# Performance work log

Measured on AMD Instinct MI355X. Metric: run time of the kernel, lower is better.

The kernel has to match this reference:

```python
import jax, jax.numpy as jnp
import numpy as np

N, M, D = 256, 64, 1024


def _l2norm(x, axis=-1, eps=1e-12):
    # tf.math.l2_normalize semantics: x / sqrt(max(sum(x^2), eps))
    sq = jnp.sum(x * x, axis=axis, keepdims=True)
    return x * jax.lax.rsqrt(jnp.maximum(sq, eps))


def setup_inputs() -> dict:
    key = jax.random.key(0)
    k1, = jax.random.split(key, 1)
    inputs = jax.random.normal(k1, (N * M, D), dtype=jnp.float32)
    w = jnp.full((1,), 10.0, dtype=jnp.float32)
    b = jnp.full((1,), -5.0, dtype=jnp.float32)
    return {"inputs": inputs, "w": w, "b": b}


def reference(inputs, w, b):
    emb = inputs.reshape(N, M, D)                       # (N, M, D)
    # speaker centroids (normalized mean over utterances)
    center = _l2norm(jnp.mean(emb, axis=1))             # (N, D)
    # leave-one-out centroid per utterance: sum over M minus self (NOT divided)
    center_except = _l2norm(jnp.sum(emb, axis=1, keepdims=True) - emb)  # (N, M, D)
    # off-diagonal similarities: every utterance vs every speaker centroid
    sim_all = jnp.einsum('jmd,id->jmi', emb, center)    # (N_utt_spk j, M, N_centroid i)
    # diagonal (i == j): utterance vs its own leave-one-out centroid
    diag = jnp.sum(center_except * emb, axis=-1)        # (N, M)
    eye = jnp.eye(N, dtype=bool)[:, None, :]            # (N, 1, N)
    sim = jnp.where(eye, diag[:, :, None], sim_all)     # (N, M, N)
    sim = w * sim + b
    return sim.reshape(N * M, N)
```

## Files before the change

### kernel.cpp

```cpp
#include <hip/hip_runtime.h>

#define NSPK 256
#define MUTT 64
#define DDIM 1024
#define NROW (NSPK * MUTT)

using frag_ab = __attribute__((ext_vector_type(8))) short;
using frag_cd = __attribute__((ext_vector_type(4))) float;

static __device__ __forceinline__ unsigned short f32_to_bf16(float f) {
    unsigned int u = __float_as_uint(f);
    return (unsigned short)((u + 0x7FFFu + ((u >> 16) & 1u)) >> 16);
}
static __device__ __forceinline__ unsigned int pack2(float a, float b) {
    return (unsigned)f32_to_bf16(a) | ((unsigned)f32_to_bf16(b) << 16);
}
static __device__ __forceinline__ void gload16(const void* g, void* l) {
    __builtin_amdgcn_global_load_lds(
        (const __attribute__((address_space(1))) unsigned int*)g,
        (__attribute__((address_space(3))) unsigned int*)l, 16, 0, 0);
}


__global__ void __launch_bounds__(512) k_prep(const float* __restrict__ emb,
                                              unsigned short* __restrict__ ebf,
                                              unsigned short* __restrict__ cbf,
                                              float* __restrict__ qg,
                                              float* __restrict__ n2g,
                                              float* __restrict__ n1g) {
    const int j = blockIdx.x;
    const int t = threadIdx.x;
    const int cg = t & 255;
    const int half = t >> 8;
    const int lane = t & 63, wave = t >> 6;
    const size_t rb = (size_t)j * MUTT + (size_t)half * 32;
    const float* src = emb + rb * DDIM + (size_t)cg * 4;
    unsigned short* edst = ebf + rb * DDIM + (size_t)cg * 4;
    __shared__ float qws[64][4];
    __shared__ float4 csum[256];
    __shared__ float red[4];
    __shared__ float sc_sh;
    float4 s = make_float4(0.f, 0.f, 0.f, 0.f);
    #pragma unroll 8
    for (int m = 0; m < 32; ++m) {
        float4 v = *(const float4*)(src + (size_t)m * DDIM);
        s.x += v.x; s.y += v.y; s.z += v.z; s.w += v.w;
        float qp = v.x * v.x + v.y * v.y + v.z * v.z + v.w * v.w;
        #pragma unroll
        for (int off = 32; off > 0; off >>= 1) qp += __shfl_down(qp, off, 64);
        if (lane == 0) qws[half * 32 + m][wave & 3] = qp;
        *(uint2*)(edst + (size_t)m * DDIM) = make_uint2(pack2(v.x, v.y), pack2(v.z, v.w));
    }
    if (half) csum[cg] = s;
    __syncthreads();
    if (t < 64) qg[(size_t)j * MUTT + t] = qws[t][0] + qws[t][1] + qws[t][2] + qws[t][3];
    if (!half) {
        float4 c = csum[cg];
        s.x += c.x; s.y += c.y; s.z += c.z; s.w += c.w;
        float sq = s.x * s.x + s.y * s.y + s.z * s.z + s.w * s.w;
        #pragma unroll
        for (int off = 32; off > 0; off >>= 1) sq += __shfl_down(sq, off, 64);
        if (lane == 0) red[wave] = sq;
    }
    __syncthreads();
    if (t == 0) {
        float tot = red[0] + red[1] + red[2] + red[3];
        n2g[j] = tot;
        n1g[j] = sqrtf(tot);
        float msq = tot * (1.0f / 4096.0f);
        sc_sh = rsqrtf(fmaxf(msq, 1e-12f)) * (1.0f / 64.0f);
    }
    __syncthreads();
    if (!half) {
        const float sc = sc_sh;
        *(uint2*)(cbf + (size_t)j * DDIM + (size_t)cg * 4) =
            make_uint2(pack2(s.x * sc, s.y * sc), pack2(s.z * sc, s.w * sc));
    }
}

__global__ void __launch_bounds__(256)
k_gemm(const unsigned short* __restrict__ ebf, const unsigned short* __restrict__ cbf,
       const float* __restrict__ qg, const float* __restrict__ n2g,
       const float* __restrict__ n1g,
       const float* __restrict__ wp, const float* __restrict__ bp,
       float* __restrict__ out) {
    __shared__ unsigned short lds[2 * 32768];

    const int tid = threadIdx.x, lane = tid & 63, wave = tid >> 6;
    const int rt = blockIdx.x;
    const int ct = blockIdx.y;
    const int row0 = rt * 128, c0 = ct * 128;

    int goff[8];
    #pragma unroll
    for (int i = 0; i < 8; ++i) {
        int c = i * 256 + tid, row = c >> 4, sw = c & 15;
        goff[i] = row * (DDIM * 2) + ((sw ^ (row & 15)) << 4);
    }
    const int stsh = wave * 512;
    const char* ag = (const char*)(ebf + (size_t)row0 * DDIM);
    const char* bg = (const char*)(cbf + (size_t)c0 * DDIM);

    const int quad = lane >> 4, m16 = lane & 15;
    const int wrow = wave >> 1, wcol = wave & 1;

    frag_cd acc[4][4];
    #pragma unroll
    for (int rr = 0; rr < 4; ++rr)
        #pragma unroll
        for (int cc = 0; cc < 4; ++cc) acc[rr][cc] = (frag_cd){0.f, 0.f, 0.f, 0.f};

    #pragma unroll
    for (int i = 0; i < 8; ++i) gload16(ag + goff[i], &lds[i * 2048 + stsh]);
    #pragma unroll
    for (int i = 0; i < 8; ++i) gload16(bg + goff[i], &lds[16384 + i * 2048 + stsh]);
    __syncthreads();

    const int NIT = DDIM / 128;
    for (int it = 0; it < NIT; ++it) {
        const int cur = it & 1;
        if (it + 1 < NIT) {
            const char* an = ag + (size_t)(it + 1) * 256;
            const char* bn = bg + (size_t)(it + 1) * 256;
            unsigned short* Ln = &lds[(cur ^ 1) * 32768];
            #pragma unroll
            for (int i = 0; i < 8; ++i) gload16(an + goff[i], Ln + i * 2048 + stsh);
            #pragma unroll
            for (int i = 0; i < 8; ++i) gload16(bn + goff[i], Ln + 16384 + i * 2048 + stsh);
        }
        const unsigned short* L = &lds[cur * 32768];
        #pragma unroll
        for (int s = 0; s < 4; ++s) {
            const int kc = (s << 2) + quad;
            frag_ab af[4], bf4[4];
            #pragma unroll
            for (int rr = 0; rr < 4; ++rr) {
                int r = wrow * 64 + rr * 16 + m16;
                int addr = r * 256 + ((kc ^ (r & 15)) << 4);
                af[rr] = *(const frag_ab*)&L[addr >> 1];
            }
            #pragma unroll
            for (int cc = 0; cc < 4; ++cc) {
                int r = wcol * 64 + cc * 16 + m16;
                int addr = 32768 + r * 256 + ((kc ^ (r & 15)) << 4);
                bf4[cc] = *(const frag_ab*)&L[addr >> 1];
            }
            #pragma unroll
            for (int rr = 0; rr < 4; ++rr)
                #pragma unroll
                for (int cc = 0; cc < 4; ++cc)
                    acc[rr][cc] = __builtin_amdgcn_mfma_f32_16x16x32_bf16(
                        af[rr], bf4[cc], acc[rr][cc], 0, 0, 0);
        }
        __syncthreads();
    }

    const float wv = wp[0], bv = bp[0];
    #pragma unroll
    for (int rr = 0; rr < 4; ++rr) {
        int rbase = wrow * 64 + rr * 16 + (quad << 2);
        #pragma unroll
        for (int cc = 0; cc < 4; ++cc) {
            int col = c0 + wcol * 64 + cc * 16 + m16;
            frag_cd v = acc[rr][cc];
            #pragma unroll
            for (int r2 = 0; r2 < 4; ++r2) {
                int grow = row0 + rbase + r2;
                float val = v[r2];
                int js = grow >> 6;
                if (col == js) {
                    float q = qg[grow];
                    float rd = val * n1g[js];
                    float den2 = n2g[js] - 2.f * rd + q;
                    val = (rd - q) * rsqrtf(fmaxf(den2, 1e-12f));
                }
                out[(size_t)grow * NSPK + col] = wv * val + bv;
            }
        }
    }
}


__global__ void k_sums(const float* __restrict__ emb, float* __restrict__ Sp) {
    const int j = blockIdx.x;
    const int h = blockIdx.y;
    const int c = threadIdx.x;
    const float* base = emb + ((size_t)j * MUTT + (size_t)h * 32) * DDIM + (size_t)c * 4;
    float4 acc = make_float4(0.f, 0.f, 0.f, 0.f);
    #pragma unroll 8
    for (int m = 0; m < 32; ++m) {
        float4 v = *(const float4*)(base + (size_t)m * DDIM);
        acc.x += v.x; acc.y += v.y; acc.z += v.z; acc.w += v.w;
    }
    *(float4*)(Sp + ((size_t)h * NSPK + j) * DDIM + (size_t)c * 4) = acc;
}

template <int P>
__global__ void k_center(const float* __restrict__ Sp, unsigned short* __restrict__ cbf,
                         float* __restrict__ normS2g, float* __restrict__ normSg) {
    const int j = blockIdx.x;
    const int t = threadIdx.x;
    float4 v = make_float4(0.f, 0.f, 0.f, 0.f);
    #pragma unroll
    for (int p = 0; p < P; ++p) {
        float4 a = *(const float4*)(Sp + ((size_t)p * NSPK + j) * DDIM + (size_t)t * 4);
        v.x += a.x; v.y += a.y; v.z += a.z; v.w += a.w;
    }
    float sq = v.x * v.x + v.y * v.y + v.z * v.z + v.w * v.w;
    #pragma unroll
    for (int off = 32; off > 0; off >>= 1) sq += __shfl_down(sq, off, 64);
    __shared__ float ws[4];
    __shared__ float sc_sh;
    const int lane = t & 63, wave = t >> 6;
    if (lane == 0) ws[wave] = sq;
    __syncthreads();
    if (t == 0) {
        float tot = ws[0] + ws[1] + ws[2] + ws[3];
        normS2g[j] = tot;
        normSg[j]  = sqrtf(tot);
        float msq = tot * (1.0f / 4096.0f);
        sc_sh = rsqrtf(fmaxf(msq, 1e-12f)) * (1.0f / 64.0f);
    }
    __syncthreads();
    const float sc = sc_sh;
    *(uint2*)(cbf + (size_t)j * DDIM + (size_t)t * 4) =
        make_uint2(pack2(v.x * sc, v.y * sc), pack2(v.z * sc, v.w * sc));
}

__global__ void __launch_bounds__(256)
k_gemm_old(const float* __restrict__ emb, const unsigned short* __restrict__ cbf,
           const float* __restrict__ normS2g, const float* __restrict__ normSg,
           const float* __restrict__ wp, const float* __restrict__ bp,
           float* __restrict__ out) {
    __shared__ unsigned short Asm[32][32];
    __shared__ unsigned short Bsm[256][32];
    __shared__ float qpart[32][8];
    __shared__ float qfin[32];
    const int tid = threadIdx.x, lane = tid & 63, wave = tid >> 6;
    const int row0 = blockIdx.x * 32;
    const int jspk = row0 >> 6;
    frag_cd acc[2][4];
    #pragma unroll
    for (int rr = 0; rr < 2; ++rr)
        #pragma unroll
        for (int cc = 0; cc < 4; ++cc) acc[rr][cc] = (frag_cd){0.f, 0.f, 0.f, 0.f};
    const int ar = tid >> 3, ak = (tid & 7) << 2;
    const float* aptr = emb + (size_t)(row0 + ar) * DDIM + ak;
    float qacc = 0.f;
    const int bi = tid >> 2, bk = (tid & 3) << 3;
    const int am = lane & 15, kq = (lane >> 4) << 3;
    for (int k0 = 0; k0 < DDIM; k0 += 32) {
        __syncthreads();
        float4 av = *(const float4*)(aptr + k0);
        qacc += av.x * av.x + av.y * av.y + av.z * av.z + av.w * av.w;
        *(uint2*)&Asm[ar][ak] = make_uint2(pack2(av.x, av.y), pack2(av.z, av.w));
        #pragma unroll
        for (int p = 0; p < 4; ++p) {
            int brow = p * 64 + bi;
            *(uint4*)&Bsm[brow][bk] = *(const uint4*)(cbf + (size_t)brow * DDIM + k0 + bk);
        }
        __syncthreads();
        frag_ab afr[2], bfr[4];
        #pragma unroll
        for (int rr = 0; rr < 2; ++rr) afr[rr] = *(const frag_ab*)&Asm[rr * 16 + am][kq];
        #pragma unroll
        for (int cc = 0; cc < 4; ++cc) bfr[cc] = *(const frag_ab*)&Bsm[wave * 64 + cc * 16 + am][kq];
        #pragma unroll
        for (int rr = 0; rr < 2; ++rr)
            #pragma unroll
            for (int cc = 0; cc < 4; ++cc)
                acc[rr][cc] = __builtin_amdgcn_mfma_f32_16x16x32_bf16(afr[rr], bfr[cc], acc[rr][cc], 0, 0, 0);
    }
    qpart[ar][tid & 7] = qacc;
    __syncthreads();
    if (tid < 32) {
        float s = 0.f;
        #pragma unroll
        for (int u = 0; u < 8; ++u) s += qpart[tid][u];
        qfin[tid] = s;
    }
    __syncthreads();
    const float wv = wp[0], bv = bp[0];
    const float ns2 = normS2g[jspk], ns = normSg[jspk];
    #pragma unroll
    for (int rr = 0; rr < 2; ++rr) {
        int rbase = rr * 16 + ((lane >> 4) << 2);
        #pragma unroll
        for (int cc = 0; cc < 4; ++cc) {
            int col = wave * 64 + cc * 16 + (lane & 15);
            frag_cd v = acc[rr][cc];
            #pragma unroll
            for (int r2 = 0; r2 < 4; ++r2) {
                int lrow = rbase + r2;
                float val = v[r2];
                if (col == jspk) {
                    float q = qfin[lrow];
                    float rd = val * ns;
                    float den2 = ns2 - 2.f * rd + q;
                    val = (rd - q) * rsqrtf(fmaxf(den2, 1e-12f));
                }
                out[(size_t)(row0 + lrow) * NSPK + col] = wv * val + bv;
            }
        }
    }
}

extern "C" void kernel_launch(void* const* d_in, const int* in_sizes, int n_in,
                              void* d_out, int out_size, void* d_ws, size_t ws_size,
                              hipStream_t stream) {
    const float* emb = (const float*)d_in[0];
    const float* w   = (const float*)d_in[1];
    const float* b   = (const float*)d_in[2];
    float* out = (float*)d_out;

    const size_t sz_ebf = (size_t)NROW * DDIM * 2;
    const size_t sz_cbf = (size_t)NSPK * DDIM * 2;
    const size_t sz_qg  = (size_t)NROW * 4;
    const size_t need = sz_ebf + sz_cbf + sz_qg + 2 * NSPK * 4;

    if (ws_size >= need) {
        char* p = (char*)d_ws;
        unsigned short* ebf = (unsigned short*)p; p += sz_ebf;
        unsigned short* cbf = (unsigned short*)p; p += sz_cbf;
        float* qg = (float*)p;                    p += sz_qg;
        float* n2 = (float*)p;
        float* n1 = n2 + NSPK;
        k_prep<<<NSPK, 512, 0, stream>>>(emb, ebf, cbf, qg, n2, n1);
        k_gemm<<<dim3(128, 2), 256, 0, stream>>>(ebf, cbf, qg, n2, n1, w, b, out);
    } else {
        float* Sp = (float*)d_ws;
        unsigned short* cbf = (unsigned short*)(Sp + 2 * NSPK * DDIM);
        float* n2 = (float*)(cbf + NSPK * DDIM);
        float* n1 = n2 + NSPK;
        k_sums<<<dim3(NSPK, 2), 256, 0, stream>>>(emb, Sp);
        k_center<2><<<NSPK, 256, 0, stream>>>(Sp, cbf, n2, n1);
        k_gemm_old<<<NROW / 32, 256, 0, stream>>>(emb, cbf, n2, n1, w, b, out);
    }
}
```

Baseline: 135.3 us.

## Fuse bf16 conversion of embeddings into GEMM and drop bf16 staging buffer

The prep kernel no longer writes a bf16 copy of the full embedding matrix. The GEMM now reads fp32 embeddings straight from global memory, converts them to bf16 in registers and writes them to LDS. It uses one block per speaker (64 rows × 256 columns) with 32x32x16 MFMAs and a three-stage register/LDS pipeline with explicit waitcnt. This removes a 32 MB bf16 write and its re-read, at the cost of GEMM blocks reading fp32 A (twice the bytes) and doing the conversion inside the main loop.

```diff
diff --git a/kernel.cpp b/kernel.cpp
--- a/kernel.cpp
+++ b/kernel.cpp
@@ -5,8 +5,9 @@
 #define DDIM 1024
 #define NROW (NSPK * MUTT)
 
-using frag_ab = __attribute__((ext_vector_type(8))) short;
-using frag_cd = __attribute__((ext_vector_type(4))) float;
+using frag_ab  = __attribute__((ext_vector_type(8)))  short;
+using frag_cd  = __attribute__((ext_vector_type(4)))  float;
+using frag_c16 = __attribute__((ext_vector_type(16))) float;
 
 static __device__ __forceinline__ unsigned short f32_to_bf16(float f) {
     unsigned int u = __float_as_uint(f);
@@ -22,12 +23,11 @@
 }
 
 
-__global__ void __launch_bounds__(512) k_prep(const float* __restrict__ emb,
-                                              unsigned short* __restrict__ ebf,
-                                              unsigned short* __restrict__ cbf,
-                                              float* __restrict__ qg,
-                                              float* __restrict__ n2g,
-                                              float* __restrict__ n1g) {
+__global__ void __launch_bounds__(512) k_prepc(const float* __restrict__ emb,
+                                               unsigned short* __restrict__ cbf,
+                                               float* __restrict__ qg,
+                                               float* __restrict__ n2g,
+                                               float* __restrict__ n1g) {
     const int j = blockIdx.x;
     const int t = threadIdx.x;
     const int cg = t & 255;
@@ -35,7 +35,6 @@
     const int lane = t & 63, wave = t >> 6;
     const size_t rb = (size_t)j * MUTT + (size_t)half * 32;
     const float* src = emb + rb * DDIM + (size_t)cg * 4;
-    unsigned short* edst = ebf + rb * DDIM + (size_t)cg * 4;
     __shared__ float qws[64][4];
     __shared__ float4 csum[256];
     __shared__ float red[4];
@@ -49,7 +48,6 @@
         #pragma unroll
         for (int off = 32; off > 0; off >>= 1) qp += __shfl_down(qp, off, 64);
         if (lane == 0) qws[half * 32 + m][wave & 3] = qp;
-        *(uint2*)(edst + (size_t)m * DDIM) = make_uint2(pack2(v.x, v.y), pack2(v.z, v.w));
     }
     if (half) csum[cg] = s;
     __syncthreads();
@@ -79,99 +77,121 @@
 }
 
 __global__ void __launch_bounds__(256)
-k_gemm(const unsigned short* __restrict__ ebf, const unsigned short* __restrict__ cbf,
-       const float* __restrict__ qg, const float* __restrict__ n2g,
-       const float* __restrict__ n1g,
-       const float* __restrict__ wp, const float* __restrict__ bp,
-       float* __restrict__ out) {
-    __shared__ unsigned short lds[2 * 32768];
+k_gemmf(const float* __restrict__ emb, const unsigned short* __restrict__ cbf,
+        const float* __restrict__ qg, const float* __restrict__ n2g,
+        const float* __restrict__ n1g,
+        const float* __restrict__ wp, const float* __restrict__ bp,
+        float* __restrict__ out) {
+    __shared__ unsigned short lds[3 * 20480];
 
     const int tid = threadIdx.x, lane = tid & 63, wave = tid >> 6;
-    const int rt = blockIdx.x;
-    const int ct = blockIdx.y;
-    const int row0 = rt * 128, c0 = ct * 128;
-
-    int goff[8];
-    #pragma unroll
-    for (int i = 0; i < 8; ++i) {
-        int c = i * 256 + tid, row = c >> 4, sw = c & 15;
-        goff[i] = row * (DDIM * 2) + ((sw ^ (row & 15)) << 4);
-    }
-    const int stsh = wave * 512;
-    const char* ag = (const char*)(ebf + (size_t)row0 * DDIM);
-    const char* bg = (const char*)(cbf + (size_t)c0 * DDIM);
-
-    const int quad = lane >> 4, m16 = lane & 15;
-    const int wrow = wave >> 1, wcol = wave & 1;
-
-    frag_cd acc[4][4];
-    #pragma unroll
-    for (int rr = 0; rr < 4; ++rr)
-        #pragma unroll
-        for (int cc = 0; cc < 4; ++cc) acc[rr][cc] = (frag_cd){0.f, 0.f, 0.f, 0.f};
-
-    #pragma unroll
-    for (int i = 0; i < 8; ++i) gload16(ag + goff[i], &lds[i * 2048 + stsh]);
-    #pragma unroll
-    for (int i = 0; i < 8; ++i) gload16(bg + goff[i], &lds[16384 + i * 2048 + stsh]);
-    __syncthreads();
-
-    const int NIT = DDIM / 128;
-    for (int it = 0; it < NIT; ++it) {
-        const int cur = it & 1;
-        if (it + 1 < NIT) {
-            const char* an = ag + (size_t)(it + 1) * 256;
-            const char* bn = bg + (size_t)(it + 1) * 256;
-            unsigned short* Ln = &lds[(cur ^ 1) * 32768];
-            #pragma unroll
-            for (int i = 0; i < 8; ++i) gload16(an + goff[i], Ln + i * 2048 + stsh);
-            #pragma unroll
-            for (int i = 0; i < 8; ++i) gload16(bn + goff[i], Ln + 16384 + i * 2048 + stsh);
-        }
-        const unsigned short* L = &lds[cur * 32768];
-        #pragma unroll
-        for (int s = 0; s < 4; ++s) {
-            const int kc = (s << 2) + quad;
-            frag_ab af[4], bf4[4];
-            #pragma unroll
-            for (int rr = 0; rr < 4; ++rr) {
-                int r = wrow * 64 + rr * 16 + m16;
-                int addr = r * 256 + ((kc ^ (r & 15)) << 4);
-                af[rr] = *(const frag_ab*)&L[addr >> 1];
+    const int j = blockIdx.x;
+    const int row0 = j * 64;
+
+    const int arow = tid >> 3;
+    const int ga = (tid & 7) ^ (arow & 7);
+    const float* ap0 = emb + (size_t)(row0 + arow) * DDIM + ga * 8;
+    const float* ap1 = ap0 + (size_t)32 * DDIM;
+
+    const int bbase = arow * DDIM + ga * 8;
+
+    const int l31 = lane & 31, l5 = lane >> 5;
+
+    frag_c16 acc[2][2];
+    #pragma unroll
+    for (int rr = 0; rr < 2; ++rr)
+        #pragma unroll
+        for (int cc = 0; cc < 2; ++cc)
+            #pragma unroll
+            for (int q = 0; q < 16; ++q) acc[rr][cc][q] = 0.f;
+
+    float4 rA[2][4];
+
+    auto issueS = [&](int t, float4 ra[4]) {
+        const int ko = t * 64;
+        ra[0] = *(const float4*)(ap0 + ko);
+        ra[1] = *(const float4*)(ap0 + ko + 4);
+        ra[2] = *(const float4*)(ap1 + ko);
+        ra[3] = *(const float4*)(ap1 + ko + 4);
+        unsigned short* LB = &lds[(t % 3) * 20480 + 4096];
+        #pragma unroll
+        for (int i = 0; i < 8; ++i)
+            gload16(cbf + (size_t)bbase + (size_t)i * 32 * DDIM + ko,
+                    LB + ((size_t)i * 256 + tid) * 8);
+    };
+    auto writeA = [&](int t, float4 ra[4]) {
+        unsigned short* LA = &lds[(t % 3) * 20480];
+        uint4 p0 = make_uint4(pack2(ra[0].x, ra[0].y), pack2(ra[0].z, ra[0].w),
+                              pack2(ra[1].x, ra[1].y), pack2(ra[1].z, ra[1].w));
+        uint4 p1 = make_uint4(pack2(ra[2].x, ra[2].y), pack2(ra[2].z, ra[2].w),
+                              pack2(ra[3].x, ra[3].y), pack2(ra[3].z, ra[3].w));
+        *(uint4*)&LA[(size_t)tid * 8] = p0;
+        *(uint4*)&LA[((size_t)tid + 256) * 8] = p1;
+    };
+
+    issueS(0, rA[0]);
+    issueS(1, rA[1]);
+    asm volatile("s_waitcnt vmcnt(12)" ::: "memory");
+    writeA(0, rA[0]);
+    asm volatile("s_waitcnt lgkmcnt(0)" ::: "memory");
+    __builtin_amdgcn_s_barrier();
+    __builtin_amdgcn_sched_barrier(0);
+
+    const int NIT = DDIM / 64;
+    #pragma unroll
+    for (int t = 0; t < NIT; ++t) {
+        if (t + 2 < NIT) issueS(t + 2, rA[t & 1]);
+
+        const unsigned short* L  = &lds[(t % 3) * 20480];
+        const unsigned short* LB = L + 4096;
+        #pragma unroll
+        for (int ks = 0; ks < 4; ++ks) {
+            const int kc = 2 * ks + l5;
+            frag_ab af[2], bfr[2];
+            #pragma unroll
+            for (int rr = 0; rr < 2; ++rr) {
+                int r = rr * 32 + l31;
+                af[rr] = *(const frag_ab*)&L[r * 64 + ((kc ^ (r & 7)) << 3)];
             }
             #pragma unroll
-            for (int cc = 0; cc < 4; ++cc) {
-                int r = wcol * 64 + cc * 16 + m16;
-                int addr = 32768 + r * 256 + ((kc ^ (r & 15)) << 4);
-                bf4[cc] = *(const frag_ab*)&L[addr >> 1];
+            for (int cc = 0; cc < 2; ++cc) {
+                int r = wave * 64 + cc * 32 + l31;
+                bfr[cc] = *(const frag_ab*)&LB[r * 64 + ((kc ^ (r & 7)) << 3)];
             }
             #pragma unroll
-            for (int rr = 0; rr < 4; ++rr)
+            for (int rr = 0; rr < 2; ++rr)
                 #pragma unroll
-                for (int cc = 0; cc < 4; ++cc)
-                    acc[rr][cc] = __builtin_amdgcn_mfma_f32_16x16x32_bf16(
-                        af[rr], bf4[cc], acc[rr][cc], 0, 0, 0);
-        }
-        __syncthreads();
+                for (int cc = 0; cc < 2; ++cc)
+                    acc[rr][cc] = __builtin_amdgcn_mfma_f32_32x32x16_bf16(
+                        af[rr], bfr[cc], acc[rr][cc], 0, 0, 0);
+        }
+
+        if (t < NIT - 1) {
+            if (t + 2 < NIT) asm volatile("s_waitcnt vmcnt(12)" ::: "memory");
+            else             asm volatile("s_waitcnt vmcnt(0)"  ::: "memory");
+            writeA(t + 1, rA[(t + 1) & 1]);
+            asm volatile("s_waitcnt lgkmcnt(0)" ::: "memory");
+            __builtin_amdgcn_s_barrier();
+            __builtin_amdgcn_sched_barrier(0);
+        }
     }
 
     const float wv = wp[0], bv = bp[0];
-    #pragma unroll
-    for (int rr = 0; rr < 4; ++rr) {
-        int rbase = wrow * 64 + rr * 16 + (quad << 2);
-        #pragma unroll
-        for (int cc = 0; cc < 4; ++cc) {
-            int col = c0 + wcol * 64 + cc * 16 + m16;
-            frag_cd v = acc[rr][cc];
-            #pragma unroll
-            for (int r2 = 0; r2 < 4; ++r2) {
-                int grow = row0 + rbase + r2;
-                float val = v[r2];
-                int js = grow >> 6;
-                if (col == js) {
+    const float ns2 = n2g[j], ns = n1g[j];
+    #pragma unroll
+    for (int rr = 0; rr < 2; ++rr) {
+        #pragma unroll
+        for (int cc = 0; cc < 2; ++cc) {
+            frag_c16 v = acc[rr][cc];
+            const int col = wave * 64 + cc * 32 + l31;
+            #pragma unroll
+            for (int r = 0; r < 16; ++r) {
+                int grow = row0 + rr * 32 + (r & 3) + 8 * (r >> 2) + 4 * l5;
+                float val = v[r];
+                if (col == j) {
                     float q = qg[grow];
-                    float rd = val * n1g[js];
-                    float den2 = n2g[js] - 2.f * rd + q;
+                    float rd = val * ns;
+                    float den2 = ns2 - 2.f * rd + q;
                     val = (rd - q) * rsqrtf(fmaxf(den2, 1e-12f));
                 }
                 out[(size_t)grow * NSPK + col] = wv * val + bv;
@@ -313,20 +333,18 @@
     const float* b   = (const float*)d_in[2];
     float* out = (float*)d_out;
 
-    const size_t sz_ebf = (size_t)NROW * DDIM * 2;
     const size_t sz_cbf = (size_t)NSPK * DDIM * 2;
     const size_t sz_qg  = (size_t)NROW * 4;
-    const size_t need = sz_ebf + sz_cbf + sz_qg + 2 * NSPK * 4;
+    const size_t need = sz_cbf + sz_qg + 2 * NSPK * 4;
 
     if (ws_size >= need) {
         char* p = (char*)d_ws;
-        unsigned short* ebf = (unsigned short*)p; p += sz_ebf;
         unsigned short* cbf = (unsigned short*)p; p += sz_cbf;
         float* qg = (float*)p;                    p += sz_qg;
         float* n2 = (float*)p;
         float* n1 = n2 + NSPK;
-        k_prep<<<NSPK, 512, 0, stream>>>(emb, ebf, cbf, qg, n2, n1);
-        k_gemm<<<dim3(128, 2), 256, 0, stream>>>(ebf, cbf, qg, n2, n1, w, b, out);
+        k_prepc<<<NSPK, 512, 0, stream>>>(emb, cbf, qg, n2, n1);
+        k_gemmf<<<NSPK, 256, 0, stream>>>(emb, cbf, qg, n2, n1, w, b, out);
     } else {
         float* Sp = (float*)d_ws;
         unsigned short* cbf = (unsigned short*)(Sp + 2 * NSPK * DDIM);
```

Measured after the change: 143.7 us. +6.2%, slower.
